# Performance work log

Hardware: AMD Instinct MI355X
Metric: run time of the kernel (lower is better)

The kernel has to match this reference:

```python
import jax, jax.numpy as jnp
import numpy as np

N = 100000   # nodes
E = 1600000  # edges
D = 128      # state_dim
H1 = 512
H2 = 256


def setup_inputs() -> dict:
    key = jax.random.key(0)
    ks = jax.random.split(key, 8)
    x = jax.random.normal(ks[0], (N, D), jnp.float32)
    edge_index = jax.random.randint(ks[1], (2, E), 0, N, dtype=jnp.int64)
    W_gcn = jax.random.normal(ks[2], (D, D), jnp.float32) * (1.0 / np.sqrt(D))
    b_gcn = jnp.zeros((D,), jnp.float32)
    W1 = jax.random.normal(ks[3], (D, H1), jnp.float32) * (1.0 / np.sqrt(D))
    b1 = jnp.zeros((H1,), jnp.float32)
    W2 = jax.random.normal(ks[4], (H1, H2), jnp.float32) * (1.0 / np.sqrt(H1))
    b2 = jnp.zeros((H2,), jnp.float32)
    W3 = jax.random.normal(ks[5], (H2, 1), jnp.float32) * (1.0 / np.sqrt(H2))
    b3 = jnp.zeros((1,), jnp.float32)
    return {"x": x, "edge_index": edge_index, "W_gcn": W_gcn, "b_gcn": b_gcn,
            "W1": W1, "b1": b1, "W2": W2, "b2": b2, "W3": W3, "b3": b3}


def _gcn_conv(x, edge_index, W, b):
    # PyG GCNConv: linear transform, add self-loops, symmetric deg^-1/2 norm,
    # scatter-sum messages from src to dst, add bias.
    n = x.shape[0]
    loop = jnp.arange(n, dtype=edge_index.dtype)
    src = jnp.concatenate([edge_index[0], loop])
    dst = jnp.concatenate([edge_index[1], loop])
    deg = jax.ops.segment_sum(jnp.ones_like(dst, x.dtype), dst, num_segments=n)
    dinv = jnp.where(deg > 0, jax.lax.rsqrt(jnp.maximum(deg, 1e-12)), 0.0)
    norm = dinv[src] * dinv[dst]                      # [E+N]
    h = x @ W                                         # [N, D]
    msg = h[src] * norm[:, None]                      # gather + scale
    out = jax.ops.segment_sum(msg, dst, num_segments=n)  # scatter-add
    return out + b


def reference(x, edge_index, W_gcn, b_gcn, W1, b1, W2, b2, W3, b3):
    out = jax.nn.relu(_gcn_conv(x, edge_index, W_gcn, b_gcn))
    h = out + x                                       # residual
    h = jax.nn.relu(h @ W1 + b1)
    h = jax.nn.relu(h @ W2 + b2)                      # dropout is identity in eval
    return h @ W3 + b3                                # [N, 1]
```

## Files before the change

kernel.cpp:

```cpp
#include <hip/hip_runtime.h>

#define DN  128
#define H1N 512
#define H2N 256
#define TILE_A 4096
#define BKT_MAX 6144

typedef __attribute__((ext_vector_type(8))) short short8_t;
typedef __attribute__((ext_vector_type(4))) float f32x4;

__device__ inline ushort f2bf(float f) {
  union { float f; unsigned u; } v; v.f = f;
  unsigned r = v.u + 0x7FFF + ((v.u >> 16) & 1);
  return (ushort)(r >> 16);
}
__device__ inline float asf(unsigned u) {
  union { unsigned u; float f; } v; v.u = u;
  return v.f;
}


__global__ __launch_bounds__(256) void k_bcount(const int* __restrict__ dst,
                                                int* __restrict__ bcnt, int E) {
  __shared__ int h[512];
  int t = threadIdx.x;
  for (int i = t; i < 512; i += 256) h[i] = 0;
  __syncthreads();
  int base = blockIdx.x * TILE_A;
  int cnt = E - base; if (cnt > TILE_A) cnt = TILE_A;
  for (int k = t; k < cnt; k += 256) atomicAdd(&h[dst[base + k] >> 8], 1);
  __syncthreads();
  for (int i = t; i < 512; i += 256)
    if (h[i]) atomicAdd(&bcnt[i], h[i]);
}


__global__ __launch_bounds__(512) void k_bscan(const int* __restrict__ bcnt,
                                               int* __restrict__ bbase,
                                               int* __restrict__ bcur,
                                               int* __restrict__ ro,
                                               int NB, int N, int E) {
  __shared__ int s[512];
  int t = threadIdx.x;
  int v = (t < NB) ? bcnt[t] : 0;
  s[t] = v; __syncthreads();
  for (int o = 1; o < 512; o <<= 1) {
    int a = (t >= o) ? s[t - o] : 0;
    __syncthreads();
    s[t] += a;
    __syncthreads();
  }
  if (t < NB) { bbase[t] = s[t] - v; bcur[t] = s[t] - v; }
  if (t == 0) { bbase[NB] = E; ro[N] = E; }
}


__global__ __launch_bounds__(256) void k_bucketA(const int* __restrict__ ei,
                                                 int* __restrict__ bcur,
                                                 uint2* __restrict__ pairs,
                                                 int E, int NB) {
  __shared__ int hist[512];
  __shared__ int start[512];
  __shared__ int cur[512];
  __shared__ int gbase[512];
  __shared__ uint2 lp[TILE_A];
  int t = threadIdx.x;
  int base = blockIdx.x * TILE_A;
  int cnt = E - base; if (cnt > TILE_A) cnt = TILE_A;

  for (int i = t; i < 512; i += 256) hist[i] = 0;
  __syncthreads();

  int sreg[16], dreg[16];
#pragma unroll
  for (int k = 0; k < 16; ++k) {
    int idx = t + 256 * k;
    bool v = idx < cnt;
    sreg[k] = v ? ei[base + idx] : 0;
    dreg[k] = v ? ei[E + base + idx] : -1;
    if (v) atomicAdd(&hist[dreg[k] >> 8], 1);
  }
  __syncthreads();

  for (int i = t; i < 512; i += 256) start[i] = hist[i];
  __syncthreads();
  for (int o = 1; o < 512; o <<= 1) {
    int i0 = t, i1 = t + 256;
    int v0 = (i0 >= o) ? start[i0 - o] : 0;
    int v1 = (i1 >= o) ? start[i1 - o] : 0;
    __syncthreads();
    start[i0] += v0;
    start[i1] += v1;
    __syncthreads();
  }
  for (int i = t; i < 512; i += 256) start[i] -= hist[i];
  __syncthreads();
  for (int i = t; i < 512; i += 256) cur[i] = start[i];
  __syncthreads();

#pragma unroll
  for (int k = 0; k < 16; ++k) {
    if (dreg[k] >= 0) {
      int d = dreg[k] >> 8;
      int p = atomicAdd(&cur[d], 1);
      lp[p] = make_uint2((unsigned)sreg[k], (unsigned)dreg[k]);
    }
  }
  __syncthreads();

  for (int i = t; i < NB; i += 256)
    gbase[i] = hist[i] ? atomicAdd(&bcur[i], hist[i]) : 0;
  __syncthreads();

  for (int p = t; p < cnt; p += 256) {
    uint2 pr = lp[p];
    int d = (int)(pr.y >> 8);
    pairs[gbase[d] + (p - start[d])] = pr;
  }
}


__global__ __launch_bounds__(256) void k_bucketB(const uint2* __restrict__ pairs,
                                                 const int* __restrict__ bbase,
                                                 int* __restrict__ csr,
                                                 int* __restrict__ ro,
                                                 float* __restrict__ dinv,
                                                 int N) {
  __shared__ int hist[256];
  __shared__ int cur[256];
  __shared__ int lout[BKT_MAX];
  __shared__ uint2 lp[BKT_MAX];
  int b = blockIdx.x, t = threadIdx.x;
  int p0 = bbase[b];
  int cnt = bbase[b + 1] - p0;

  hist[t] = 0;
  __syncthreads();
  for (int k = t; k < cnt; k += 256) {
    uint2 pr = pairs[p0 + k];
    if (k < BKT_MAX) lp[k] = pr;
    atomicAdd(&hist[pr.y & 255u], 1);
  }
  __syncthreads();

  int v = hist[t];
  cur[t] = v; __syncthreads();
  for (int o = 1; o < 256; o <<= 1) {
    int a = (t >= o) ? cur[t - o] : 0;
    __syncthreads();
    cur[t] += a;
    __syncthreads();
  }
  int excl = cur[t] - v;
  int node = (b << 8) + t;
  if (node < N) {
    ro[node] = p0 + excl;
    dinv[node] = rsqrtf((float)(v + 1));
  }
  __syncthreads();
  cur[t] = excl;
  __syncthreads();

  for (int k = t; k < cnt; k += 256) {
    uint2 pr = (k < BKT_MAX) ? lp[k] : pairs[p0 + k];
    int p = atomicAdd(&cur[(int)(pr.y & 255u)], 1);
    if (p < BKT_MAX) lout[p] = (int)pr.x;
    else csr[p0 + p] = (int)pr.x;
  }
  __syncthreads();
  int lim = cnt < BKT_MAX ? cnt : BKT_MAX;
  for (int k = t; k < lim; k += 256) csr[p0 + k] = lout[k];
}


__device__ inline void pack_one(int idx, const float* __restrict__ W,
                                ushort* __restrict__ Wp, int K, int Ncols) {
  int ksn = K >> 5;
  int l  = idx & 63;
  int ks = (idx >> 6) % ksn;
  int ct = idx / (64 * ksn);
  int col = ct * 16 + (l & 15);
  int kb  = ks * 32 + (l >> 4) * 8;
  short8_t v;
#pragma unroll
  for (int r = 0; r < 8; ++r)
    v[r] = (short)f2bf(W[(size_t)(kb + r) * Ncols + col]);
  *(short8_t*)&Wp[(size_t)idx * 8] = v;
}

__global__ __launch_bounds__(256) void k_packall(const float* __restrict__ Wg,
                                                 const float* __restrict__ W1,
                                                 const float* __restrict__ W2,
                                                 ushort* __restrict__ Wgp,
                                                 ushort* __restrict__ W1p,
                                                 ushort* __restrict__ W2p) {
  int idx = blockIdx.x * 256 + threadIdx.x;
  if (idx < 2048)        pack_one(idx, Wg, Wgp, DN, DN);
  else if (idx < 10240)  pack_one(idx - 2048, W1, W1p, DN, H1N);
  else if (idx < 26624)  pack_one(idx - 10240, W2, W2p, H1N, H2N);
}


__global__ __launch_bounds__(256, 4) void k_gemm1(const float* __restrict__ x,
                                                  const ushort* __restrict__ Wgp,
                                                  const float* __restrict__ dinv,
                                                  ushort* __restrict__ hs, int N) {
  __shared__ ushort xT[64 * 128];
  int t = threadIdx.x;
  int row0 = blockIdx.x * 64;

#pragma unroll
  for (int i = 0; i < 4; ++i) {
    int c = t + 256 * i;
    int r = c >> 4, d0 = (c & 15) * 8;
    int gr = row0 + r;
    float4 v0 = {0,0,0,0}, v1 = {0,0,0,0};
    if (gr < N) {
      v0 = *(const float4*)(x + (size_t)gr * DN + d0);
      v1 = *(const float4*)(x + (size_t)gr * DN + d0 + 4);
    }
    short8_t p;
    p[0]=(short)f2bf(v0.x); p[1]=(short)f2bf(v0.y); p[2]=(short)f2bf(v0.z); p[3]=(short)f2bf(v0.w);
    p[4]=(short)f2bf(v1.x); p[5]=(short)f2bf(v1.y); p[6]=(short)f2bf(v1.z); p[7]=(short)f2bf(v1.w);
    *(short8_t*)((char*)xT + r * 256 + ((d0 * 2) ^ ((r & 7) << 4))) = p;
  }
  __syncthreads();

  int w = t >> 6, l = t & 63;
  int lr = l & 15, lk = l >> 4;
  const short8_t* pbg = (const short8_t*)Wgp;

  f32x4 acc[4][2];
#pragma unroll
  for (int mf = 0; mf < 4; ++mf)
#pragma unroll
    for (int n = 0; n < 2; ++n) acc[mf][n] = (f32x4){0.f,0.f,0.f,0.f};

  auto g_load = [&](short8_t (&bb)[2], int ks) {
#pragma unroll
    for (int n = 0; n < 2; ++n)
      bb[n] = pbg[((w * 2 + n) * 4 + ks) * 64 + l];
  };
  auto g_mfma = [&](short8_t (&bb)[2], int ks) {
    short8_t a[4];
#pragma unroll
    for (int mf = 0; mf < 4; ++mf) {
      int r = mf * 16 + lr;
      a[mf] = *(const short8_t*)((const char*)xT + r * 256 + ((ks * 64 + lk * 16) ^ ((r & 7) << 4)));
    }
#pragma unroll
    for (int mf = 0; mf < 4; ++mf)
#pragma unroll
      for (int n = 0; n < 2; ++n)
        acc[mf][n] = __builtin_amdgcn_mfma_f32_16x16x32_bf16(a[mf], bb[n], acc[mf][n], 0, 0, 0);
  };

  short8_t bA[2], bB[2];
  g_load(bA, 0);
  g_load(bB, 1); g_mfma(bA, 0);
  g_load(bA, 2); g_mfma(bB, 1);
  g_load(bB, 3); g_mfma(bA, 2);
  g_mfma(bB, 3);

  float dv[4][4];
#pragma unroll
  for (int mf = 0; mf < 4; ++mf)
#pragma unroll
    for (int r2 = 0; r2 < 4; ++r2) {
      int gr = row0 + mf * 16 + lk * 4 + r2;
      dv[mf][r2] = (gr < N) ? dinv[gr] : 0.f;
    }
#pragma unroll
  for (int n = 0; n < 2; ++n) {
    int col = (w * 2 + n) * 16 + lr;
#pragma unroll
    for (int mf = 0; mf < 4; ++mf)
#pragma unroll
      for (int r2 = 0; r2 < 4; ++r2) {
        int gr = row0 + mf * 16 + lk * 4 + r2;
        if (gr < N) hs[(size_t)gr * DN + col] = f2bf(acc[mf][n][r2] * dv[mf][r2]);
      }
  }
}


__global__ __launch_bounds__(256) void k_agg(const ushort* __restrict__ hs,
                                             const float* __restrict__ x,
                                             const int* __restrict__ csr,
                                             const int* __restrict__ ro,
                                             const float* __restrict__ dinv,
                                             const float* __restrict__ bg,
                                             ushort* __restrict__ aggb, int N) {
  int t = threadIdx.x;
  int node = blockIdx.x * 16 + (t >> 4);
  if (node >= N) return;
  int d0 = (t & 15) * 8;

  int beg = ro[node], end = ro[node + 1];
  float dn = dinv[node];
  uint4 selfv = *(const uint4*)(hs + (size_t)node * DN + d0);
  float4 x0 = *(const float4*)(x + (size_t)node * DN + d0);
  float4 x1 = *(const float4*)(x + (size_t)node * DN + d0 + 4);
  float4 b0 = *(const float4*)(bg + d0);
  float4 b1v = *(const float4*)(bg + d0 + 4);

  float s[8];
#pragma unroll
  for (int i = 0; i < 8; ++i) s[i] = 0.f;

  auto accum = [&](uint4 v) {
    s[0] += asf(v.x << 16); s[1] += asf(v.x & 0xffff0000u);
    s[2] += asf(v.y << 16); s[3] += asf(v.y & 0xffff0000u);
    s[4] += asf(v.z << 16); s[5] += asf(v.z & 0xffff0000u);
    s[6] += asf(v.w << 16); s[7] += asf(v.w & 0xffff0000u);
  };

  int e = beg;
  for (; e + 4 <= end; e += 4) {
    int i0 = csr[e], i1 = csr[e + 1], i2 = csr[e + 2], i3 = csr[e + 3];
    uint4 v0 = *(const uint4*)(hs + (size_t)i0 * DN + d0);
    uint4 v1 = *(const uint4*)(hs + (size_t)i1 * DN + d0);
    uint4 v2 = *(const uint4*)(hs + (size_t)i2 * DN + d0);
    uint4 v3 = *(const uint4*)(hs + (size_t)i3 * DN + d0);
    accum(v0); accum(v1); accum(v2); accum(v3);
  }
  if (e + 2 <= end) {
    int i0 = csr[e], i1 = csr[e + 1];
    uint4 v0 = *(const uint4*)(hs + (size_t)i0 * DN + d0);
    uint4 v1 = *(const uint4*)(hs + (size_t)i1 * DN + d0);
    accum(v0); accum(v1);
    e += 2;
  }
  if (e < end) {
    int i0 = csr[e];
    accum(*(const uint4*)(hs + (size_t)i0 * DN + d0));
  }
  accum(selfv);

  float xv[8] = {x0.x, x0.y, x0.z, x0.w, x1.x, x1.y, x1.z, x1.w};
  float bv[8] = {b0.x, b0.y, b0.z, b0.w, b1v.x, b1v.y, b1v.z, b1v.w};
  uint outp[4];
#pragma unroll
  for (int i = 0; i < 4; ++i) {
    ushort lo = f2bf(fmaxf(s[2*i]   * dn + bv[2*i],   0.f) + xv[2*i]);
    ushort hi = f2bf(fmaxf(s[2*i+1] * dn + bv[2*i+1], 0.f) + xv[2*i+1]);
    outp[i] = (uint)lo | ((uint)hi << 16);
  }
  *(uint4*)(aggb + (size_t)node * DN + d0) = *(uint4*)outp;
}


__global__ __launch_bounds__(256, 2) void k_mlp(const ushort* __restrict__ aggb,
                                                const ushort* __restrict__ W1p,
                                                const float* __restrict__ b1,
                                                const ushort* __restrict__ W2p,
                                                const float* __restrict__ b2,
                                                const float* __restrict__ W3,
                                                const float* __restrict__ b3,
                                                float* __restrict__ out, int N) {
  __shared__ ushort aT[64 * 128];
  __shared__ ushort t1[64 * 512];
  int t = threadIdx.x;
  int row0 = blockIdx.x * 64;

#pragma unroll
  for (int i = 0; i < 4; ++i) {
    int c = t + 256 * i;
    int r = c >> 4;
    int cb = (c & 15) * 16;
    int gr = row0 + r;
    uint4 v = {0, 0, 0, 0};
    if (gr < N) v = *(const uint4*)(aggb + (size_t)gr * DN + (c & 15) * 8);
    *(uint4*)((char*)aT + r * 256 + (cb ^ ((r & 7) << 4))) = v;
  }
  __syncthreads();

  int w = t >> 6, l = t & 63;
  int lr = l & 15, lk = l >> 4;

  const short8_t* pb1 = (const short8_t*)W1p;
  f32x4 acc1[4][8];
#pragma unroll
  for (int mf = 0; mf < 4; ++mf)
#pragma unroll
    for (int n = 0; n < 8; ++n) acc1[mf][n] = (f32x4){0.f,0.f,0.f,0.f};

  auto s1_load = [&](short8_t (&bb)[8], int ks) {
#pragma unroll
    for (int n = 0; n < 8; ++n)
      bb[n] = pb1[((w * 8 + n) * 4 + ks) * 64 + l];
  };
  auto s1_mfma = [&](short8_t (&bb)[8], int ks) {
    short8_t a[4];
#pragma unroll
    for (int mf = 0; mf < 4; ++mf) {
      int r = mf * 16 + lr;
      a[mf] = *(const short8_t*)((const char*)aT + r * 256 + ((ks * 64 + lk * 16) ^ ((r & 7) << 4)));
    }
#pragma unroll
    for (int mf = 0; mf < 4; ++mf)
#pragma unroll
      for (int n = 0; n < 8; ++n)
        acc1[mf][n] = __builtin_amdgcn_mfma_f32_16x16x32_bf16(a[mf], bb[n], acc1[mf][n], 0, 0, 0);
  };

  {
    short8_t bA[8], bB[8];
    s1_load(bA, 0);
    s1_load(bB, 1); s1_mfma(bA, 0);
    s1_load(bA, 2); s1_mfma(bB, 1);
    s1_load(bB, 3); s1_mfma(bA, 2);
    s1_mfma(bB, 3);
  }

#pragma unroll
  for (int n = 0; n < 8; ++n) {
    int col = (w * 8 + n) * 16 + lr;
    float bb = b1[col];
#pragma unroll
    for (int mf = 0; mf < 4; ++mf)
#pragma unroll
      for (int r2 = 0; r2 < 4; ++r2) {
        int rr = mf * 16 + lk * 4 + r2;
        *(ushort*)((char*)t1 + rr * 1024 + ((col * 2) ^ ((rr & 7) << 4))) =
            f2bf(fmaxf(acc1[mf][n][r2] + bb, 0.f));
      }
  }
  __syncthreads();

  const short8_t* pb2 = (const short8_t*)W2p;
  f32x4 acc2[4][4];
#pragma unroll
  for (int mf = 0; mf < 4; ++mf)
#pragma unroll
    for (int n = 0; n < 4; ++n) acc2[mf][n] = (f32x4){0.f,0.f,0.f,0.f};

  auto s2_load = [&](short8_t (&bb)[8], int p) {
#pragma unroll
    for (int n = 0; n < 4; ++n) {
      bb[n]     = pb2[((w * 4 + n) * 16 + 2 * p)     * 64 + l];
      bb[4 + n] = pb2[((w * 4 + n) * 16 + 2 * p + 1) * 64 + l];
    }
  };
  auto s2_mfma = [&](short8_t (&bb)[8], int p) {
#pragma unroll
    for (int h = 0; h < 2; ++h) {
      int ks = 2 * p + h;
      short8_t a[4];
#pragma unroll
      for (int mf = 0; mf < 4; ++mf) {
        int r = mf * 16 + lr;
        a[mf] = *(const short8_t*)((const char*)t1 + r * 1024 + ((ks * 64 + lk * 16) ^ ((r & 7) << 4)));
      }
#pragma unroll
      for (int mf = 0; mf < 4; ++mf)
#pragma unroll
        for (int n = 0; n < 4; ++n)
          acc2[mf][n] = __builtin_amdgcn_mfma_f32_16x16x32_bf16(a[mf], bb[h * 4 + n], acc2[mf][n], 0, 0, 0);
    }
  };

  {
    short8_t c0[8], c1[8], c2[8];
    s2_load(c0, 0); s2_load(c1, 1);
    s2_load(c2, 2); s2_mfma(c0, 0);
    s2_load(c0, 3); s2_mfma(c1, 1);
    s2_load(c1, 4); s2_mfma(c2, 2);
    s2_load(c2, 5); s2_mfma(c0, 3);
    s2_load(c0, 6); s2_mfma(c1, 4);
    s2_load(c1, 7); s2_mfma(c2, 5);
    s2_mfma(c0, 6);
    s2_mfma(c1, 7);
  }

  float po[4][4];
#pragma unroll
  for (int mf = 0; mf < 4; ++mf)
#pragma unroll
    for (int r2 = 0; r2 < 4; ++r2) po[mf][r2] = 0.f;
#pragma unroll
  for (int n = 0; n < 4; ++n) {
    int col = (w * 4 + n) * 16 + lr;
    float bb = b2[col];
    float w3 = W3[col];
#pragma unroll
    for (int mf = 0; mf < 4; ++mf)
#pragma unroll
      for (int r2 = 0; r2 < 4; ++r2)
        po[mf][r2] += fmaxf(acc2[mf][n][r2] + bb, 0.f) * w3;
  }
#pragma unroll
  for (int mf = 0; mf < 4; ++mf)
#pragma unroll
    for (int r2 = 0; r2 < 4; ++r2) {
      float v = po[mf][r2];
      v += __shfl_xor(v, 1, 64);
      v += __shfl_xor(v, 2, 64);
      v += __shfl_xor(v, 4, 64);
      v += __shfl_xor(v, 8, 64);
      po[mf][r2] = v;
    }
  float* pf = (float*)aT;
  if (lr == 0) {
#pragma unroll
    for (int mf = 0; mf < 4; ++mf)
#pragma unroll
      for (int r2 = 0; r2 < 4; ++r2)
        pf[w * 64 + mf * 16 + lk * 4 + r2] = po[mf][r2];
  }
  __syncthreads();
  if (t < 64) {
    int gr = row0 + t;
    if (gr < N)
      out[gr] = pf[t] + pf[64 + t] + pf[128 + t] + pf[192 + t] + b3[0];
  }
}


extern "C" void kernel_launch(void* const* d_in, const int* in_sizes, int n_in,
                              void* d_out, int out_size, void* d_ws, size_t ws_size,
                              hipStream_t stream) {
  const float* x  = (const float*)d_in[0];
  const int*   ei = (const int*)d_in[1];
  const float* Wg = (const float*)d_in[2];
  const float* bg = (const float*)d_in[3];
  const float* W1 = (const float*)d_in[4];
  const float* b1 = (const float*)d_in[5];
  const float* W2 = (const float*)d_in[6];
  const float* b2 = (const float*)d_in[7];
  const float* W3 = (const float*)d_in[8];
  const float* b3 = (const float*)d_in[9];
  float* out = (float*)d_out;

  const int N = in_sizes[0] / DN;
  const int E = in_sizes[1] / 2;
  const int NB = (N + 255) >> 8;

  char* ws = (char*)d_ws;
  size_t off = 0;
  auto alloc = [&](size_t bytes) -> void* {
    void* p = ws + off;
    off = (off + bytes + 255) & ~(size_t)255;
    return p;
  };
  int*    bcnt   = (int*)alloc((size_t)NB * 4);
  int*    bbase  = (int*)alloc(((size_t)NB + 1) * 4);
  int*    bcur   = (int*)alloc((size_t)NB * 4);
  int*    ro     = (int*)alloc(((size_t)N + 1) * 4);
  float*  dinv   = (float*)alloc((size_t)N * 4);
  int*    csr    = (int*)alloc((size_t)E * 4);
  uint2*  pairs  = (uint2*)alloc((size_t)E * 8);
  ushort* hsb    = (ushort*)alloc((size_t)N * DN * 2);
  ushort* aggb   = (ushort*)alloc((size_t)N * DN * 2);
  ushort* Wgp    = (ushort*)alloc((size_t)DN * DN * 2);
  ushort* W1p    = (ushort*)alloc((size_t)DN * H1N * 2);
  ushort* W2p    = (ushort*)alloc((size_t)H1N * H2N * 2);
  (void)ws_size; (void)n_in; (void)out_size;

  hipMemsetAsync(bcnt, 0, (size_t)NB * 4, stream);

  int nTiles = (E + TILE_A - 1) / TILE_A;
  k_bcount<<<nTiles, 256, 0, stream>>>(ei + E, bcnt, E);
  k_bscan<<<1, 512, 0, stream>>>(bcnt, bbase, bcur, ro, NB, N, E);
  k_bucketA<<<nTiles, 256, 0, stream>>>(ei, bcur, pairs, E, NB);
  k_bucketB<<<NB, 256, 0, stream>>>(pairs, bbase, csr, ro, dinv, N);

  k_packall<<<104, 256, 0, stream>>>(Wg, W1, W2, Wgp, W1p, W2p);

  int nb64 = (N + 63) / 64;
  k_gemm1<<<nb64, 256, 0, stream>>>(x, Wgp, dinv, hsb, N);
  k_agg<<<(N + 15) / 16, 256, 0, stream>>>(hsb, x, csr, ro, dinv, bg, aggb, N);
  k_mlp<<<nb64, 256, 0, stream>>>(aggb, W1p, b1, W2p, b2, W3, b3, out, N);
}
```

Before: 200.6 us.

## Split aggregation into two half-feature passes and widen MLP tiles to 128 rows

```diff
diff --git a/kernel.cpp b/kernel.cpp
--- a/kernel.cpp
+++ b/kernel.cpp
@@ -290,67 +290,61 @@
                                              const int* __restrict__ ro,
                                              const float* __restrict__ dinv,
                                              const float* __restrict__ bg,
-                                             ushort* __restrict__ aggb, int N) {
+                                             ushort* __restrict__ aggb,
+                                             int dbase, int N) {
   int t = threadIdx.x;
   int node = blockIdx.x * 16 + (t >> 4);
   if (node >= N) return;
-  int d0 = (t & 15) * 8;
+  int d0 = dbase + (t & 15) * 4;
 
   int beg = ro[node], end = ro[node + 1];
   float dn = dinv[node];
-  uint4 selfv = *(const uint4*)(hs + (size_t)node * DN + d0);
-  float4 x0 = *(const float4*)(x + (size_t)node * DN + d0);
-  float4 x1 = *(const float4*)(x + (size_t)node * DN + d0 + 4);
-  float4 b0 = *(const float4*)(bg + d0);
-  float4 b1v = *(const float4*)(bg + d0 + 4);
-
-  float s[8];
-#pragma unroll
-  for (int i = 0; i < 8; ++i) s[i] = 0.f;
-
-  auto accum = [&](uint4 v) {
-    s[0] += asf(v.x << 16); s[1] += asf(v.x & 0xffff0000u);
-    s[2] += asf(v.y << 16); s[3] += asf(v.y & 0xffff0000u);
-    s[4] += asf(v.z << 16); s[5] += asf(v.z & 0xffff0000u);
-    s[6] += asf(v.w << 16); s[7] += asf(v.w & 0xffff0000u);
+  uint2 selfv = *(const uint2*)(hs + (size_t)node * DN + d0);
+  float4 xv = *(const float4*)(x + (size_t)node * DN + d0);
+  float4 bv = *(const float4*)(bg + d0);
+
+  float s0 = 0.f, s1 = 0.f, s2 = 0.f, s3 = 0.f;
+  auto accum = [&](uint2 v) {
+    s0 += asf(v.x << 16); s1 += asf(v.x & 0xffff0000u);
+    s2 += asf(v.y << 16); s3 += asf(v.y & 0xffff0000u);
   };
 
   int e = beg;
   for (; e + 4 <= end; e += 4) {
     int i0 = csr[e], i1 = csr[e + 1], i2 = csr[e + 2], i3 = csr[e + 3];
-    uint4 v0 = *(const uint4*)(hs + (size_t)i0 * DN + d0);
-    uint4 v1 = *(const uint4*)(hs + (size_t)i1 * DN + d0);
-    uint4 v2 = *(const uint4*)(hs + (size_t)i2 * DN + d0);
-    uint4 v3 = *(const uint4*)(hs + (size_t)i3 * DN + d0);
+    uint2 v0 = *(const uint2*)(hs + (size_t)i0 * DN + d0);
+    uint2 v1 = *(const uint2*)(hs + (size_t)i1 * DN + d0);
+    uint2 v2 = *(const uint2*)(hs + (size_t)i2 * DN + d0);
+    uint2 v3 = *(const uint2*)(hs + (size_t)i3 * DN + d0);
     accum(v0); accum(v1); accum(v2); accum(v3);
   }
   if (e + 2 <= end) {
     int i0 = csr[e], i1 = csr[e + 1];
-    uint4 v0 = *(const uint4*)(hs + (size_t)i0 * DN + d0);
-    uint4 v1 = *(const uint4*)(hs + (size_t)i1 * DN + d0);
+    uint2 v0 = *(const uint2*)(hs + (size_t)i0 * DN + d0);
+    uint2 v1 = *(const uint2*)(hs + (size_t)i1 * DN + d0);
     accum(v0); accum(v1);
     e += 2;
   }
   if (e < end) {
     int i0 = csr[e];
-    accum(*(const uint4*)(hs + (size_t)i0 * DN + d0));
+    accum(*(const uint2*)(hs + (size_t)i0 * DN + d0));
   }
   accum(selfv);
 
-  float xv[8] = {x0.x, x0.y, x0.z, x0.w, x1.x, x1.y, x1.z, x1.w};
-  float bv[8] = {b0.x, b0.y, b0.z, b0.w, b1v.x, b1v.y, b1v.z, b1v.w};
-  uint outp[4];
-#pragma unroll
-  for (int i = 0; i < 4; ++i) {
-    ushort lo = f2bf(fmaxf(s[2*i]   * dn + bv[2*i],   0.f) + xv[2*i]);
-    ushort hi = f2bf(fmaxf(s[2*i+1] * dn + bv[2*i+1], 0.f) + xv[2*i+1]);
-    outp[i] = (uint)lo | ((uint)hi << 16);
-  }
-  *(uint4*)(aggb + (size_t)node * DN + d0) = *(uint4*)outp;
-}
-
-
-__global__ __launch_bounds__(256, 2) void k_mlp(const ushort* __restrict__ aggb,
+  uint outp[2];
+  {
+    ushort lo = f2bf(fmaxf(s0 * dn + bv.x, 0.f) + xv.x);
+    ushort hi = f2bf(fmaxf(s1 * dn + bv.y, 0.f) + xv.y);
+    outp[0] = (uint)lo | ((uint)hi << 16);
+    lo = f2bf(fmaxf(s2 * dn + bv.z, 0.f) + xv.z);
+    hi = f2bf(fmaxf(s3 * dn + bv.w, 0.f) + xv.w);
+    outp[1] = (uint)lo | ((uint)hi << 16);
+  }
+  *(uint2*)(aggb + (size_t)node * DN + d0) = *(uint2*)outp;
+}
+
+
+__global__ __launch_bounds__(512, 2) void k_mlp(const ushort* __restrict__ aggb,
                                                 const ushort* __restrict__ W1p,
                                                 const float* __restrict__ b1,
                                                 const ushort* __restrict__ W2p,
@@ -359,109 +353,108 @@
                                                 const float* __restrict__ b3,
                                                 float* __restrict__ out, int N) {
   __shared__ ushort aT[64 * 128];
-  __shared__ ushort t1[64 * 512];
+  __shared__ ushort t1[128 * 512];
   int t = threadIdx.x;
-  int row0 = blockIdx.x * 64;
-
-#pragma unroll
-  for (int i = 0; i < 4; ++i) {
-    int c = t + 256 * i;
-    int r = c >> 4;
-    int cb = (c & 15) * 16;
-    int gr = row0 + r;
-    uint4 v = {0, 0, 0, 0};
-    if (gr < N) v = *(const uint4*)(aggb + (size_t)gr * DN + (c & 15) * 8);
-    *(uint4*)((char*)aT + r * 256 + (cb ^ ((r & 7) << 4))) = v;
-  }
-  __syncthreads();
-
+  int row0 = blockIdx.x * 128;
   int w = t >> 6, l = t & 63;
   int lr = l & 15, lk = l >> 4;
 
   const short8_t* pb1 = (const short8_t*)W1p;
-  f32x4 acc1[4][8];
-#pragma unroll
-  for (int mf = 0; mf < 4; ++mf)
-#pragma unroll
-    for (int n = 0; n < 8; ++n) acc1[mf][n] = (f32x4){0.f,0.f,0.f,0.f};
-
-  auto s1_load = [&](short8_t (&bb)[8], int ks) {
-#pragma unroll
-    for (int n = 0; n < 8; ++n)
-      bb[n] = pb1[((w * 8 + n) * 4 + ks) * 64 + l];
-  };
-  auto s1_mfma = [&](short8_t (&bb)[8], int ks) {
-    short8_t a[4];
+  short8_t b1f[4][4];
+#pragma unroll
+  for (int n = 0; n < 4; ++n)
+#pragma unroll
+    for (int ks = 0; ks < 4; ++ks)
+      b1f[n][ks] = pb1[((w * 4 + n) * 4 + ks) * 64 + l];
+  float b1c[4];
+#pragma unroll
+  for (int n = 0; n < 4; ++n) b1c[n] = b1[(w * 4 + n) * 16 + lr];
+
+  auto stage_aT = [&](int h) {
+#pragma unroll
+    for (int i = 0; i < 2; ++i) {
+      int c = t + 512 * i;
+      int r = c >> 4, d0 = (c & 15) * 8;
+      int gr = row0 + h * 64 + r;
+      uint4 v = {0, 0, 0, 0};
+      if (gr < N) v = *(const uint4*)(aggb + (size_t)gr * DN + d0);
+      *(uint4*)((char*)aT + r * 256 + ((d0 * 2) ^ ((r & 7) << 4))) = v;
+    }
+  };
+
+  stage_aT(0);
+  __syncthreads();
+#pragma unroll
+  for (int h = 0; h < 2; ++h) {
+    if (h) {
+      __syncthreads();
+      stage_aT(1);
+      __syncthreads();
+    }
 #pragma unroll
     for (int mf = 0; mf < 4; ++mf) {
-      int r = mf * 16 + lr;
-      a[mf] = *(const short8_t*)((const char*)aT + r * 256 + ((ks * 64 + lk * 16) ^ ((r & 7) << 4)));
-    }
-#pragma unroll
-    for (int mf = 0; mf < 4; ++mf)
-#pragma unroll
-      for (int n = 0; n < 8; ++n)
-        acc1[mf][n] = __builtin_amdgcn_mfma_f32_16x16x32_bf16(a[mf], bb[n], acc1[mf][n], 0, 0, 0);
-  };
-
-  {
-    short8_t bA[8], bB[8];
-    s1_load(bA, 0);
-    s1_load(bB, 1); s1_mfma(bA, 0);
-    s1_load(bA, 2); s1_mfma(bB, 1);
-    s1_load(bB, 3); s1_mfma(bA, 2);
-    s1_mfma(bB, 3);
-  }
-
-#pragma unroll
-  for (int n = 0; n < 8; ++n) {
-    int col = (w * 8 + n) * 16 + lr;
-    float bb = b1[col];
-#pragma unroll
-    for (int mf = 0; mf < 4; ++mf)
-#pragma unroll
-      for (int r2 = 0; r2 < 4; ++r2) {
-        int rr = mf * 16 + lk * 4 + r2;
-        *(ushort*)((char*)t1 + rr * 1024 + ((col * 2) ^ ((rr & 7) << 4))) =
-            f2bf(fmaxf(acc1[mf][n][r2] + bb, 0.f));
+      short8_t a[4];
+#pragma unroll
+      for (int ks = 0; ks < 4; ++ks) {
+        int r = mf * 16 + lr;
+        a[ks] = *(const short8_t*)((const char*)aT + r * 256 + ((ks * 64 + lk * 16) ^ ((r & 7) << 4)));
       }
+      f32x4 acc[4];
+#pragma unroll
+      for (int n = 0; n < 4; ++n) acc[n] = (f32x4){0.f,0.f,0.f,0.f};
+#pragma unroll
+      for (int ks = 0; ks < 4; ++ks)
+#pragma unroll
+        for (int n = 0; n < 4; ++n)
+          acc[n] = __builtin_amdgcn_mfma_f32_16x16x32_bf16(a[ks], b1f[n][ks], acc[n], 0, 0, 0);
+#pragma unroll
+      for (int n = 0; n < 4; ++n) {
+        int col = (w * 4 + n) * 16 + lr;
+#pragma unroll
+        for (int r2 = 0; r2 < 4; ++r2) {
+          int rr = h * 64 + mf * 16 + lk * 4 + r2;
+          *(ushort*)((char*)t1 + rr * 1024 + ((col * 2) ^ ((rr & 7) << 4))) =
+              f2bf(fmaxf(acc[n][r2] + b1c[n], 0.f));
+        }
+      }
+    }
   }
   __syncthreads();
 
   const short8_t* pb2 = (const short8_t*)W2p;
-  f32x4 acc2[4][4];
-#pragma unroll
-  for (int mf = 0; mf < 4; ++mf)
-#pragma unroll
-    for (int n = 0; n < 4; ++n) acc2[mf][n] = (f32x4){0.f,0.f,0.f,0.f};
-
-  auto s2_load = [&](short8_t (&bb)[8], int p) {
-#pragma unroll
-    for (int n = 0; n < 4; ++n) {
-      bb[n]     = pb2[((w * 4 + n) * 16 + 2 * p)     * 64 + l];
-      bb[4 + n] = pb2[((w * 4 + n) * 16 + 2 * p + 1) * 64 + l];
-    }
-  };
-  auto s2_mfma = [&](short8_t (&bb)[8], int p) {
-#pragma unroll
-    for (int h = 0; h < 2; ++h) {
-      int ks = 2 * p + h;
-      short8_t a[4];
-#pragma unroll
-      for (int mf = 0; mf < 4; ++mf) {
+  f32x4 acc2[8][2];
+#pragma unroll
+  for (int mf = 0; mf < 8; ++mf)
+#pragma unroll
+    for (int n = 0; n < 2; ++n) acc2[mf][n] = (f32x4){0.f,0.f,0.f,0.f};
+
+  auto s2_load = [&](short8_t (&bb)[4], int p) {
+#pragma unroll
+    for (int n = 0; n < 2; ++n) {
+      bb[n]     = pb2[((w * 2 + n) * 16 + 2 * p)     * 64 + l];
+      bb[2 + n] = pb2[((w * 2 + n) * 16 + 2 * p + 1) * 64 + l];
+    }
+  };
+  auto s2_mfma = [&](short8_t (&bb)[4], int p) {
+#pragma unroll
+    for (int h2 = 0; h2 < 2; ++h2) {
+      int ks = 2 * p + h2;
+      short8_t a[8];
+#pragma unroll
+      for (int mf = 0; mf < 8; ++mf) {
         int r = mf * 16 + lr;
         a[mf] = *(const short8_t*)((const char*)t1 + r * 1024 + ((ks * 64 + lk * 16) ^ ((r & 7) << 4)));
       }
 #pragma unroll
-      for (int mf = 0; mf < 4; ++mf)
-#pragma unroll
-        for (int n = 0; n < 4; ++n)
-          acc2[mf][n] = __builtin_amdgcn_mfma_f32_16x16x32_bf16(a[mf], bb[h * 4 + n], acc2[mf][n], 0, 0, 0);
+      for (int mf = 0; mf < 8; ++mf)
+#pragma unroll
+        for (int n = 0; n < 2; ++n)
+          acc2[mf][n] = __builtin_amdgcn_mfma_f32_16x16x32_bf16(a[mf], bb[2 * h2 + n], acc2[mf][n], 0, 0, 0);
     }
   };
 
   {
-    short8_t c0[8], c1[8], c2[8];
+    short8_t c0[4], c1[4], c2[4];
     s2_load(c0, 0); s2_load(c1, 1);
     s2_load(c2, 2); s2_mfma(c0, 0);
     s2_load(c0, 3); s2_mfma(c1, 1);
@@ -473,24 +466,24 @@
     s2_mfma(c1, 7);
   }
 
-  float po[4][4];
-#pragma unroll
-  for (int mf = 0; mf < 4; ++mf)
+  float po[8][4];
+#pragma unroll
+  for (int mf = 0; mf < 8; ++mf)
 #pragma unroll
     for (int r2 = 0; r2 < 4; ++r2) po[mf][r2] = 0.f;
 #pragma unroll
-  for (int n = 0; n < 4; ++n) {
-    int col = (w * 4 + n) * 16 + lr;
+  for (int n = 0; n < 2; ++n) {
+    int col = (w * 2 + n) * 16 + lr;
     float bb = b2[col];
     float w3 = W3[col];
 #pragma unroll
-    for (int mf = 0; mf < 4; ++mf)
+    for (int mf = 0; mf < 8; ++mf)
 #pragma unroll
       for (int r2 = 0; r2 < 4; ++r2)
         po[mf][r2] += fmaxf(acc2[mf][n][r2] + bb, 0.f) * w3;
   }
 #pragma unroll
-  for (int mf = 0; mf < 4; ++mf)
+  for (int mf = 0; mf < 8; ++mf)
 #pragma unroll
     for (int r2 = 0; r2 < 4; ++r2) {
       float v = po[mf][r2];
@@ -503,16 +496,20 @@
   float* pf = (float*)aT;
   if (lr == 0) {
 #pragma unroll
-    for (int mf = 0; mf < 4; ++mf)
+    for (int mf = 0; mf < 8; ++mf)
 #pragma unroll
       for (int r2 = 0; r2 < 4; ++r2)
-        pf[w * 64 + mf * 16 + lk * 4 + r2] = po[mf][r2];
-  }
-  __syncthreads();
-  if (t < 64) {
+        pf[w * 128 + mf * 16 + lk * 4 + r2] = po[mf][r2];
+  }
+  __syncthreads();
+  if (t < 128) {
     int gr = row0 + t;
-    if (gr < N)
-      out[gr] = pf[t] + pf[64 + t] + pf[128 + t] + pf[192 + t] + b3[0];
+    if (gr < N) {
+      float s = b3[0];
+#pragma unroll
+      for (int ww = 0; ww < 8; ++ww) s += pf[ww * 128 + t];
+      out[gr] = s;
+    }
   }
 }
 
@@ -569,6 +566,8 @@
 
   int nb64 = (N + 63) / 64;
   k_gemm1<<<nb64, 256, 0, stream>>>(x, Wgp, dinv, hsb, N);
-  k_agg<<<(N + 15) / 16, 256, 0, stream>>>(hsb, x, csr, ro, dinv, bg, aggb, N);
-  k_mlp<<<nb64, 256, 0, stream>>>(aggb, W1p, b1, W2p, b2, W3, b3, out, N);
-}
+  k_agg<<<(N + 15) / 16, 256, 0, stream>>>(hsb, x, csr, ro, dinv, bg, aggb, 0, N);
+  k_agg<<<(N + 15) / 16, 256, 0, stream>>>(hsb, x, csr, ro, dinv, bg, aggb, 64, N);
+  int nb128 = (N + 127) / 128;
+  k_mlp<<<nb128, 512, 0, stream>>>(aggb, W1p, b1, W2p, b2, W3, b3, out, N);
+}
```

New measurement: 216.9 us. +8.1%, slower.

## Fuse neighbor aggregation into MLP kernel, writing aggregated rows straight to LDS

Applied to the files above, without the earlier changes.

```diff
diff --git a/kernel.cpp b/kernel.cpp
--- a/kernel.cpp
+++ b/kernel.cpp
@@ -284,94 +284,81 @@
 }
 
 
-__global__ __launch_bounds__(256) void k_agg(const ushort* __restrict__ hs,
-                                             const float* __restrict__ x,
-                                             const int* __restrict__ csr,
-                                             const int* __restrict__ ro,
-                                             const float* __restrict__ dinv,
-                                             const float* __restrict__ bg,
-                                             ushort* __restrict__ aggb, int N) {
-  int t = threadIdx.x;
-  int node = blockIdx.x * 16 + (t >> 4);
-  if (node >= N) return;
-  int d0 = (t & 15) * 8;
-
-  int beg = ro[node], end = ro[node + 1];
-  float dn = dinv[node];
-  uint4 selfv = *(const uint4*)(hs + (size_t)node * DN + d0);
-  float4 x0 = *(const float4*)(x + (size_t)node * DN + d0);
-  float4 x1 = *(const float4*)(x + (size_t)node * DN + d0 + 4);
-  float4 b0 = *(const float4*)(bg + d0);
-  float4 b1v = *(const float4*)(bg + d0 + 4);
-
-  float s[8];
-#pragma unroll
-  for (int i = 0; i < 8; ++i) s[i] = 0.f;
-
-  auto accum = [&](uint4 v) {
-    s[0] += asf(v.x << 16); s[1] += asf(v.x & 0xffff0000u);
-    s[2] += asf(v.y << 16); s[3] += asf(v.y & 0xffff0000u);
-    s[4] += asf(v.z << 16); s[5] += asf(v.z & 0xffff0000u);
-    s[6] += asf(v.w << 16); s[7] += asf(v.w & 0xffff0000u);
-  };
-
-  int e = beg;
-  for (; e + 4 <= end; e += 4) {
-    int i0 = csr[e], i1 = csr[e + 1], i2 = csr[e + 2], i3 = csr[e + 3];
-    uint4 v0 = *(const uint4*)(hs + (size_t)i0 * DN + d0);
-    uint4 v1 = *(const uint4*)(hs + (size_t)i1 * DN + d0);
-    uint4 v2 = *(const uint4*)(hs + (size_t)i2 * DN + d0);
-    uint4 v3 = *(const uint4*)(hs + (size_t)i3 * DN + d0);
-    accum(v0); accum(v1); accum(v2); accum(v3);
-  }
-  if (e + 2 <= end) {
-    int i0 = csr[e], i1 = csr[e + 1];
-    uint4 v0 = *(const uint4*)(hs + (size_t)i0 * DN + d0);
-    uint4 v1 = *(const uint4*)(hs + (size_t)i1 * DN + d0);
-    accum(v0); accum(v1);
-    e += 2;
-  }
-  if (e < end) {
-    int i0 = csr[e];
-    accum(*(const uint4*)(hs + (size_t)i0 * DN + d0));
-  }
-  accum(selfv);
-
-  float xv[8] = {x0.x, x0.y, x0.z, x0.w, x1.x, x1.y, x1.z, x1.w};
-  float bv[8] = {b0.x, b0.y, b0.z, b0.w, b1v.x, b1v.y, b1v.z, b1v.w};
-  uint outp[4];
-#pragma unroll
-  for (int i = 0; i < 4; ++i) {
-    ushort lo = f2bf(fmaxf(s[2*i]   * dn + bv[2*i],   0.f) + xv[2*i]);
-    ushort hi = f2bf(fmaxf(s[2*i+1] * dn + bv[2*i+1], 0.f) + xv[2*i+1]);
-    outp[i] = (uint)lo | ((uint)hi << 16);
-  }
-  *(uint4*)(aggb + (size_t)node * DN + d0) = *(uint4*)outp;
-}
-
-
-__global__ __launch_bounds__(256, 2) void k_mlp(const ushort* __restrict__ aggb,
-                                                const ushort* __restrict__ W1p,
-                                                const float* __restrict__ b1,
-                                                const ushort* __restrict__ W2p,
-                                                const float* __restrict__ b2,
-                                                const float* __restrict__ W3,
-                                                const float* __restrict__ b3,
-                                                float* __restrict__ out, int N) {
+__global__ __launch_bounds__(256, 2) void k_aggmlp(const ushort* __restrict__ hs,
+                                                   const float* __restrict__ x,
+                                                   const int* __restrict__ csr,
+                                                   const int* __restrict__ ro,
+                                                   const float* __restrict__ dinv,
+                                                   const float* __restrict__ bg,
+                                                   const ushort* __restrict__ W1p,
+                                                   const float* __restrict__ b1,
+                                                   const ushort* __restrict__ W2p,
+                                                   const float* __restrict__ b2,
+                                                   const float* __restrict__ W3,
+                                                   const float* __restrict__ b3,
+                                                   float* __restrict__ out, int N) {
   __shared__ ushort aT[64 * 128];
   __shared__ ushort t1[64 * 512];
   int t = threadIdx.x;
   int row0 = blockIdx.x * 64;
 
 #pragma unroll
-  for (int i = 0; i < 4; ++i) {
-    int c = t + 256 * i;
-    int r = c >> 4;
-    int cb = (c & 15) * 16;
-    int gr = row0 + r;
-    uint4 v = {0, 0, 0, 0};
-    if (gr < N) v = *(const uint4*)(aggb + (size_t)gr * DN + (c & 15) * 8);
-    *(uint4*)((char*)aT + r * 256 + (cb ^ ((r & 7) << 4))) = v;
+  for (int pass = 0; pass < 4; ++pass) {
+    int r = pass * 16 + (t >> 4);
+    int node = row0 + r;
+    int d0 = (t & 15) * 8;
+    uint outp[4] = {0u, 0u, 0u, 0u};
+    if (node < N) {
+      int beg = ro[node], end = ro[node + 1];
+      float dn = dinv[node];
+      uint4 selfv = *(const uint4*)(hs + (size_t)node * DN + d0);
+      float4 x0 = *(const float4*)(x + (size_t)node * DN + d0);
+      float4 x1 = *(const float4*)(x + (size_t)node * DN + d0 + 4);
+      float4 bb0 = *(const float4*)(bg + d0);
+      float4 bb1 = *(const float4*)(bg + d0 + 4);
+
+      float s[8];
+#pragma unroll
+      for (int i = 0; i < 8; ++i) s[i] = 0.f;
+      auto accum = [&](uint4 v) {
+        s[0] += asf(v.x << 16); s[1] += asf(v.x & 0xffff0000u);
+        s[2] += asf(v.y << 16); s[3] += asf(v.y & 0xffff0000u);
+        s[4] += asf(v.z << 16); s[5] += asf(v.z & 0xffff0000u);
+        s[6] += asf(v.w << 16); s[7] += asf(v.w & 0xffff0000u);
+      };
+
+      int e = beg;
+      for (; e + 4 <= end; e += 4) {
+        int i0 = csr[e], i1 = csr[e + 1], i2 = csr[e + 2], i3 = csr[e + 3];
+        uint4 v0 = *(const uint4*)(hs + (size_t)i0 * DN + d0);
+        uint4 v1 = *(const uint4*)(hs + (size_t)i1 * DN + d0);
+        uint4 v2 = *(const uint4*)(hs + (size_t)i2 * DN + d0);
+        uint4 v3 = *(const uint4*)(hs + (size_t)i3 * DN + d0);
+        accum(v0); accum(v1); accum(v2); accum(v3);
+      }
+      if (e + 2 <= end) {
+        int i0 = csr[e], i1 = csr[e + 1];
+        uint4 v0 = *(const uint4*)(hs + (size_t)i0 * DN + d0);
+        uint4 v1 = *(const uint4*)(hs + (size_t)i1 * DN + d0);
+        accum(v0); accum(v1);
+        e += 2;
+      }
+      if (e < end) {
+        int i0 = csr[e];
+        accum(*(const uint4*)(hs + (size_t)i0 * DN + d0));
+      }
+      accum(selfv);
+
+      float xv[8] = {x0.x, x0.y, x0.z, x0.w, x1.x, x1.y, x1.z, x1.w};
+      float bv[8] = {bb0.x, bb0.y, bb0.z, bb0.w, bb1.x, bb1.y, bb1.z, bb1.w};
+#pragma unroll
+      for (int i = 0; i < 4; ++i) {
+        ushort lo = f2bf(fmaxf(s[2*i]   * dn + bv[2*i],   0.f) + xv[2*i]);
+        ushort hi = f2bf(fmaxf(s[2*i+1] * dn + bv[2*i+1], 0.f) + xv[2*i+1]);
+        outp[i] = (uint)lo | ((uint)hi << 16);
+      }
+    }
+    *(uint4*)((char*)aT + r * 256 + ((d0 * 2) ^ ((r & 7) << 4))) = *(uint4*)outp;
   }
   __syncthreads();
 
@@ -551,7 +538,6 @@
   int*    csr    = (int*)alloc((size_t)E * 4);
   uint2*  pairs  = (uint2*)alloc((size_t)E * 8);
   ushort* hsb    = (ushort*)alloc((size_t)N * DN * 2);
-  ushort* aggb   = (ushort*)alloc((size_t)N * DN * 2);
   ushort* Wgp    = (ushort*)alloc((size_t)DN * DN * 2);
   ushort* W1p    = (ushort*)alloc((size_t)DN * H1N * 2);
   ushort* W2p    = (ushort*)alloc((size_t)H1N * H2N * 2);
@@ -569,6 +555,6 @@
 
   int nb64 = (N + 63) / 64;
   k_gemm1<<<nb64, 256, 0, stream>>>(x, Wgp, dinv, hsb, N);
-  k_agg<<<(N + 15) / 16, 256, 0, stream>>>(hsb, x, csr, ro, dinv, bg, aggb, N);
-  k_mlp<<<nb64, 256, 0, stream>>>(aggb, W1p, b1, W2p, b2, W3, b3, out, N);
-}
+  k_aggmlp<<<nb64, 256, 0, stream>>>(hsb, x, csr, ro, dinv, bg,
+                                     W1p, b1, W2p, b2, W3, b3, out, N);
+}
```

Result: slower. 216.9 us (+8.1%).
